# Kernel tuning notes

Measured on AMD Instinct MI355X. Metric: run time of the kernel, lower is better.

The kernel has to match this reference:

```python
import jax, jax.numpy as jnp
import numpy as np

B, S, H = 1, 4096, 2048
NH, NKV, HD = 8, 4, 256
I = 8192
EPS = 1e-6
THETA = 10000.0
WINDOW = 4096  # hardcoded sliding window for even layer_idx
LAYER_IDX = 0


def rms_norm(x, w):
    v = jnp.mean(jnp.square(x), axis=-1, keepdims=True)
    return x * jax.lax.rsqrt(v + EPS) * w


def rotate_half(x):
    h = x.shape[-1] // 2
    return jnp.concatenate([-x[..., h:], x[..., :h]], axis=-1)


def apply_rope(q, k, positions):
    # q: [B,S,NH,HD], k: [B,S,NKV,HD], positions: [B,S]
    inv_freq = 1.0 / (THETA ** (jnp.arange(0, HD, 2, dtype=jnp.float32) / HD))
    freqs = positions.astype(jnp.float32)[..., None] * inv_freq  # [B,S,HD/2]
    emb = jnp.concatenate([freqs, freqs], axis=-1)               # [B,S,HD]
    cos = jnp.cos(emb)[:, :, None, :]
    sin = jnp.sin(emb)[:, :, None, :]
    q = q * cos + rotate_half(q) * sin
    k = k * cos + rotate_half(k) * sin
    return q, k


def forward(hidden_states, q_w, k_w, v_w, o_w, gate_w, up_w, down_w, ln1_w, ln2_w,
            attention_mask, position_ids):
    # ---- input RMSNorm + attention ----
    residual = hidden_states
    x = rms_norm(hidden_states, ln1_w)

    q = (x @ q_w).reshape(B, S, NH, HD)
    k = (x @ k_w).reshape(B, S, NKV, HD)
    v = (x @ v_w).reshape(B, S, NKV, HD)
    q, k = apply_rope(q, k, position_ids)

    # GQA: repeat kv heads to match query heads
    groups = NH // NKV
    k = jnp.repeat(k, groups, axis=2)  # [B,S,NH,HD]
    v = jnp.repeat(v, groups, axis=2)

    # masks: padding mask AND causal AND (even layer) local window of WINDOW
    row = jnp.arange(S)[:, None]
    col = jnp.arange(S)[None, :]
    causal = col <= row                                   # [S,S]
    combined = causal[None, None] & (attention_mask[:, None, None, :] > 0)
    if LAYER_IDX % 2 == 0:
        keep = ~(col <= row - WINDOW)                     # mask out keys older than WINDOW
        combined = combined & keep[None, None]
    neg = jnp.finfo(jnp.float32).min
    bias = jnp.where(combined, 0.0, neg).astype(jnp.float32)  # [B,1,S,S]

    scale = HD ** -0.5
    scores = jnp.einsum('bqhd,bkhd->bhqk', q, k) * scale + bias
    probs = jax.nn.softmax(scores, axis=-1)
    attn = jnp.einsum('bhqk,bkhd->bqhd', probs, v).reshape(B, S, NH * HD)
    attn_out = attn @ o_w

    hidden_states = residual + attn_out

    # ---- post-attention RMSNorm + gated-GeLU MLP ----
    residual = hidden_states
    x = rms_norm(hidden_states, ln2_w)
    mlp = (jax.nn.gelu(x @ gate_w, approximate=True) * (x @ up_w)) @ down_w
    return residual + mlp


def setup_inputs() -> dict:
    key = jax.random.key(0)
    ks = jax.random.split(key, 9)
    std = 0.02
    n = lambda k, shp: jax.random.normal(k, shp, dtype=jnp.float32) * std
    return {
        'hidden_states': jax.random.normal(ks[0], (B, S, H), dtype=jnp.float32),
        'q_w': n(ks[1], (H, NH * HD)),
        'k_w': n(ks[2], (H, NKV * HD)),
        'v_w': n(ks[3], (H, NKV * HD)),
        'o_w': n(ks[4], (NH * HD, H)),
        'gate_w': n(ks[5], (H, I)),
        'up_w': n(ks[6], (H, I)),
        'down_w': n(ks[7], (I, H)),
        'ln1_w': jnp.ones((H,), jnp.float32),
        'ln2_w': jnp.ones((H,), jnp.float32),
        'attention_mask': jnp.ones((B, S), jnp.int32),
        'position_ids': jnp.broadcast_to(jnp.arange(S, dtype=jnp.int32)[None, :], (B, S)),
    }


def reference(hidden_states, q_w, k_w, v_w, o_w, gate_w, up_w, down_w, ln1_w, ln2_w,
              attention_mask, position_ids):
    return forward(hidden_states, q_w, k_w, v_w, o_w, gate_w, up_w, down_w,
                   ln1_w, ln2_w, attention_mask, position_ids)
```

## Files before the change

kernel.cpp:

```cpp
#include <hip/hip_runtime.h>
#include <hip/hip_bf16.h>
#include <math.h>

#define S_LEN 4096
#define HID   2048
#define NHEADS 8
#define NKVH   4
#define HDIM   256
#define FFN    8192
#define WIN    4096

typedef __bf16 bf16_t;
typedef __bf16 bf16x4 __attribute__((ext_vector_type(4)));
typedef __bf16 bf16x8 __attribute__((ext_vector_type(8)));
typedef float  floatx4 __attribute__((ext_vector_type(4)));

__device__ inline float waveReduceSum(float v) {
#pragma unroll
    for (int o = 32; o > 0; o >>= 1) v += __shfl_xor(v, o);
    return v;
}
__device__ inline float blockReduceSum(float v, float* sh) {
    int tid = threadIdx.x;
    v = waveReduceSum(v);
    if ((tid & 63) == 0) sh[tid >> 6] = v;
    __syncthreads();
    v = sh[0] + sh[1] + sh[2] + sh[3];
    __syncthreads();
    return v;
}

template <typename T>
__global__ __launch_bounds__(256) void transpose_bf16_kernel(const T* __restrict__ in,
                                                             bf16_t* __restrict__ out,
                                                             int R, int C) {
    __shared__ float tile[32][33];
    int tx = threadIdx.x & 31;
    int ty = threadIdx.x >> 5;
    int c0 = blockIdx.x * 32;
    int r0 = blockIdx.y * 32;
#pragma unroll
    for (int i = 0; i < 4; ++i)
        tile[ty + i * 8][tx] = (float)in[(long long)(r0 + ty + i * 8) * C + c0 + tx];
    __syncthreads();
#pragma unroll
    for (int i = 0; i < 4; ++i)
        out[(long long)(c0 + ty + i * 8) * R + r0 + tx] = (bf16_t)tile[tx][ty + i * 8];
}

__global__ __launch_bounds__(256) void rmsnorm_kernel(const float* __restrict__ x,
                                                      const float* __restrict__ w,
                                                      bf16_t* __restrict__ out) {
    __shared__ float sh[4];
    int row = blockIdx.x;
    const float* xr = x + (long long)row * HID;
    float v[8];
    float ss = 0.f;
#pragma unroll
    for (int i = 0; i < 8; ++i) {
        v[i] = xr[threadIdx.x + i * 256];
        ss += v[i] * v[i];
    }
    ss = blockReduceSum(ss, sh);
    float sc = rsqrtf(ss * (1.0f / HID) + 1e-6f);
#pragma unroll
    for (int i = 0; i < 8; ++i) {
        int c = threadIdx.x + i * 256;
        out[(long long)row * HID + c] = (bf16_t)(v[i] * sc * w[c]);
    }
}

__global__ __launch_bounds__(256) void rope_kernel(bf16_t* __restrict__ q,
                                                   bf16_t* __restrict__ k,
                                                   const int* __restrict__ pos_ids) {
    int s = blockIdx.x;
    float p = (float)pos_ids[s];
    for (int t = threadIdx.x; t < (NHEADS + NKVH) * (HDIM / 2); t += 256) {
        int head = t >> 7;
        int i = t & 127;
        float inv = expf(-(2.0f * (float)i / (float)HDIM) * 9.210340371976184f);
        float f = p * inv;
        float sn, cs;
        sincosf(f, &sn, &cs);
        bf16_t* base = (head < NHEADS) ? (q + (long long)s * HID + head * HDIM)
                                       : (k + (long long)s * (NKVH * HDIM) + (head - NHEADS) * HDIM);
        float a = (float)base[i];
        float b = (float)base[i + 128];
        base[i]       = (bf16_t)(a * cs - b * sn);
        base[i + 128] = (bf16_t)(b * cs + a * sn);
    }
}

__global__ __launch_bounds__(256) void flash_attn_kernel(const bf16_t* __restrict__ qg,
                                                         const bf16_t* __restrict__ kg,
                                                         const bf16_t* __restrict__ vTg,
                                                         bf16_t* __restrict__ op0,
                                                         bf16_t* __restrict__ op1,
                                                         float* __restrict__ mlb,
                                                         const int* __restrict__ amask) {
    __shared__ bf16_t sK[64 * 256];
    __shared__ bf16_t sV[256 * 64];

    const int h = blockIdx.y;
    const int kh = blockIdx.z;
    const int tid = threadIdx.x;
    const int lane = tid & 63;
    const int w = tid >> 6;
    const int tl = lane & 15;
    const int quad = lane >> 4;

    const bf16_t* Qh = qg + h * HDIM;
    const bf16_t* Kh = kg + (h >> 1) * HDIM;
    const bf16_t* Vh = vTg + (long long)(h >> 1) * HDIM * S_LEN;
    bf16_t* Op = kh ? op1 : op0;
    bf16_t* sP = sK + w * (16 * 72);

#pragma unroll 1
    for (int half = 0; half < 2; ++half) {
        const int qi = half ? (63 - blockIdx.x) : blockIdx.x;
        const int qr0 = qi * 64;
        const int ntiles = qi + 1;
        const int mid = ntiles >> 1;
        const int t0 = kh ? mid : 0;
        const int t1 = kh ? ntiles : mid;
        const int irow = qr0 + w * 16 + tl;

        const bf16_t* qrow = Qh + (long long)irow * HID;
        bf16x8 qf[8];
#pragma unroll
        for (int ks = 0; ks < 8; ++ks)
            qf[ks] = *(const bf16x8*)(qrow + (ks * 4 + quad) * 8);

        floatx4 oacc[16] = {};
        float m_i = -3e38f, l_i = 0.f;

        for (int t = t0; t < t1; ++t) {
            const int kt = t * 64;
#pragma unroll
            for (int it = 0; it < 8; ++it) {
                int s = it * 256 + tid;
                {
                    int m = s >> 5, sg = s & 31, g = sg ^ (m & 7);
                    const bf16_t* src = Kh + (long long)(kt + m) * (NKVH * HDIM) + g * 8;
                    __builtin_amdgcn_global_load_lds((const __attribute__((address_space(1))) void*)src,
                                                     (__attribute__((address_space(3))) void*)(sK + s * 8),
                                                     16, 0, 0);
                }
                {
                    int m = s >> 3, sg = s & 7, g = sg ^ (m & 7);
                    const bf16_t* src = Vh + (long long)m * S_LEN + kt + g * 8;
                    __builtin_amdgcn_global_load_lds((const __attribute__((address_space(1))) void*)src,
                                                     (__attribute__((address_space(3))) void*)(sV + s * 8),
                                                     16, 0, 0);
                }
            }
            __builtin_amdgcn_s_waitcnt(0x0f70);
            __syncthreads();

            floatx4 sacc[4] = {};
#pragma unroll
            for (int ks = 0; ks < 8; ++ks) {
                bf16x8 kf[4];
#pragma unroll
                for (int ni = 0; ni < 4; ++ni) {
                    int row = ni * 16 + tl;
                    int ph = (ks * 4 + quad) ^ (row & 7);
                    kf[ni] = *(const bf16x8*)(sK + row * 256 + ph * 8);
                }
#pragma unroll
                for (int ni = 0; ni < 4; ++ni)
                    sacc[ni] = __builtin_amdgcn_mfma_f32_16x16x32_bf16(kf[ni], qf[ks], sacc[ni], 0, 0, 0);
            }
            __syncthreads();

            float sv[4][4];
            float mx = -3e38f;
#pragma unroll
            for (int ni = 0; ni < 4; ++ni) {
                int4 am = *(const int4*)(amask + kt + ni * 16 + quad * 4);
#pragma unroll
                for (int r = 0; r < 4; ++r) {
                    int j = kt + ni * 16 + quad * 4 + r;
                    int amr = (r == 0) ? am.x : (r == 1) ? am.y : (r == 2) ? am.z : am.w;
                    bool valid = (j <= irow) && (j > irow - WIN) && (amr > 0);
                    float x = valid ? sacc[ni][r] * 0.0625f : -3e38f;
                    sv[ni][r] = x;
                    mx = fmaxf(mx, x);
                }
            }
            mx = fmaxf(mx, __shfl_xor(mx, 16));
            mx = fmaxf(mx, __shfl_xor(mx, 32));
            float mnew = fmaxf(m_i, mx);
            float alpha = __expf(m_i - mnew);
            float rs = 0.f;
#pragma unroll
            for (int ni = 0; ni < 4; ++ni) {
                bf16x4 pk;
#pragma unroll
                for (int r = 0; r < 4; ++r) {
                    float p = (sv[ni][r] > -1e37f) ? __expf(sv[ni][r] - mnew) : 0.f;
                    rs += p;
                    pk[r] = (bf16_t)p;
                }
                *(bf16x4*)(sP + tl * 72 + ni * 16 + quad * 4) = pk;
            }
            rs += __shfl_xor(rs, 16);
            rs += __shfl_xor(rs, 32);
            l_i = l_i * alpha + rs;
            m_i = mnew;

            floatx4 av;
#pragma unroll
            for (int r = 0; r < 4; ++r) av[r] = __shfl(alpha, quad * 4 + r);
#pragma unroll
            for (int dt = 0; dt < 16; ++dt) oacc[dt] *= av;

#pragma unroll
            for (int k2 = 0; k2 < 2; ++k2) {
                bf16x8 pf = *(const bf16x8*)(sP + tl * 72 + k2 * 32 + quad * 8);
#pragma unroll
                for (int dt = 0; dt < 16; ++dt) {
                    int d = dt * 16 + tl;
                    int ph = (k2 * 4 + quad) ^ (d & 7);
                    bf16x8 vf = *(const bf16x8*)(sV + d * 64 + ph * 8);
                    oacc[dt] = __builtin_amdgcn_mfma_f32_16x16x32_bf16(pf, vf, oacc[dt], 0, 0, 0);
                }
            }
            __syncthreads();
        }

        floatx4 inv;
#pragma unroll
        for (int r = 0; r < 4; ++r) {
            float lv = __shfl(l_i, quad * 4 + r);
            inv[r] = (lv > 0.f) ? 1.0f / lv : 0.f;
        }
#pragma unroll
        for (int dt = 0; dt < 16; ++dt) {
#pragma unroll
            for (int r = 0; r < 4; ++r) {
                long long row = qr0 + w * 16 + quad * 4 + r;
                Op[row * HID + h * HDIM + dt * 16 + tl] = (bf16_t)(oacc[dt][r] * inv[r]);
            }
        }
        if (quad == 0) {
            long long mi = ((long long)(kh * NHEADS + h) * S_LEN + qr0 + w * 16 + tl) * 2;
            mlb[mi] = m_i;
            mlb[mi + 1] = l_i;
        }
    }
}

__global__ __launch_bounds__(256) void combine_kernel(bf16_t* __restrict__ op0,
                                                      const bf16_t* __restrict__ op1,
                                                      const float* __restrict__ mlb) {
    int h = blockIdx.x;
    int row = blockIdx.y;
    int d = threadIdx.x;
    long long m0i = ((long long)h * S_LEN + row) * 2;
    long long m1i = ((long long)(NHEADS + h) * S_LEN + row) * 2;
    float m0 = mlb[m0i], l0 = mlb[m0i + 1];
    float m1 = mlb[m1i], l1 = mlb[m1i + 1];
    float M = fmaxf(m0, m1);
    float w0 = (l0 > 0.f) ? l0 * __expf(m0 - M) : 0.f;
    float w1 = (l1 > 0.f) ? l1 * __expf(m1 - M) : 0.f;
    float inv = 1.0f / (w0 + w1);
    long long idx = (long long)row * HID + h * HDIM + d;
    float v = (w0 * (float)op0[idx] + w1 * (float)op1[idx]) * inv;
    op0[idx] = (bf16_t)v;
}

template <int MODE>
__global__ __launch_bounds__(256) void gemm_kernel(const bf16_t* __restrict__ A, int lda,
                                                   const bf16_t* __restrict__ Bt, int ldb,
                                                   void* __restrict__ Cv, int ldc,
                                                   const void* __restrict__ aux, int K) {
    __shared__ bf16_t smem[2 * 128 * 64];
    bf16_t* sA = smem;
    bf16_t* sB = smem + 128 * 64;

    const int tid = threadIdx.x;
    const int n0 = blockIdx.x * 128;
    const int m0 = blockIdx.y * 128;

    const int lane = tid & 63;
    const int wid = tid >> 6;
    const int wm = (wid >> 1) * 64;
    const int wn = (wid & 1) * 64;
    const int tl = lane & 15;
    const int quad = lane >> 4;

    floatx4 acc[4][4] = {};

    for (int k0 = 0; k0 < K; k0 += 64) {
#pragma unroll
        for (int it = 0; it < 4; ++it) {
            int s = it * 256 + tid;
            int m = s >> 3;
            int sg = s & 7;
            int g = sg ^ (m & 7);
            const bf16_t* ga = A + (long long)(m0 + m) * lda + k0 + g * 8;
            __builtin_amdgcn_global_load_lds((const __attribute__((address_space(1))) void*)ga,
                                             (__attribute__((address_space(3))) void*)(sA + s * 8),
                                             16, 0, 0);
            const bf16_t* gb = Bt + (long long)(n0 + m) * ldb + k0 + g * 8;
            __builtin_amdgcn_global_load_lds((const __attribute__((address_space(1))) void*)gb,
                                             (__attribute__((address_space(3))) void*)(sB + s * 8),
                                             16, 0, 0);
        }
        __builtin_amdgcn_s_waitcnt(0x0f70);
        __syncthreads();

#pragma unroll
        for (int kk = 0; kk < 2; ++kk) {
            bf16x8 af[4], bfr[4];
#pragma unroll
            for (int mi = 0; mi < 4; ++mi) {
                int m = wm + mi * 16 + tl;
                int sg = (kk * 4 + quad) ^ (m & 7);
                af[mi] = *(const bf16x8*)(sA + m * 64 + sg * 8);
            }
#pragma unroll
            for (int ni = 0; ni < 4; ++ni) {
                int n = wn + ni * 16 + tl;
                int sg = (kk * 4 + quad) ^ (n & 7);
                bfr[ni] = *(const bf16x8*)(sB + n * 64 + sg * 8);
            }
#pragma unroll
            for (int mi = 0; mi < 4; ++mi)
#pragma unroll
                for (int ni = 0; ni < 4; ++ni)
                    acc[mi][ni] = __builtin_amdgcn_mfma_f32_16x16x32_bf16(af[mi], bfr[ni], acc[mi][ni], 0, 0, 0);
        }
        __syncthreads();
    }

#pragma unroll
    for (int mi = 0; mi < 4; ++mi) {
#pragma unroll
        for (int ni = 0; ni < 4; ++ni) {
#pragma unroll
            for (int r = 0; r < 4; ++r) {
                int gr = m0 + wm + mi * 16 + quad * 4 + r;
                int gc = n0 + wn + ni * 16 + tl;
                long long idx = (long long)gr * ldc + gc;
                float v = acc[mi][ni][r];
                if (MODE == 0) {
                    ((bf16_t*)Cv)[idx] = (bf16_t)v;
                } else if (MODE == 1) {
                    ((float*)Cv)[idx] = ((const float*)aux)[idx] + v;
                } else {
                    float g = (float)((const bf16_t*)aux)[idx];
                    float t = 0.7978845608028654f * (g + 0.044715f * g * g * g);
                    float ge = 0.5f * g * (1.0f + tanhf(t));
                    ((bf16_t*)Cv)[idx] = (bf16_t)(ge * v);
                }
            }
        }
    }
}

extern "C" void kernel_launch(void* const* d_in, const int* in_sizes, int n_in,
                              void* d_out, int out_size, void* d_ws, size_t ws_size,
                              hipStream_t stream) {
    const float* hidden = (const float*)d_in[0];
    const float* q_w    = (const float*)d_in[1];
    const float* k_w    = (const float*)d_in[2];
    const float* v_w    = (const float*)d_in[3];
    const float* o_w    = (const float*)d_in[4];
    const float* gate_w = (const float*)d_in[5];
    const float* up_w   = (const float*)d_in[6];
    const float* down_w = (const float*)d_in[7];
    const float* ln1_w  = (const float*)d_in[8];
    const float* ln2_w  = (const float*)d_in[9];
    const int* amask    = (const int*)d_in[10];
    const int* pos_ids  = (const int*)d_in[11];
    float* out = (float*)d_out;

    const size_t MB = 1ull << 20;
    char* ws = (char*)d_ws;
    bf16_t* wqT = (bf16_t*)(ws + 0 * MB);
    bf16_t* wkT = (bf16_t*)(ws + 8 * MB);
    bf16_t* wvT = (bf16_t*)(ws + 12 * MB);
    bf16_t* woT = (bf16_t*)(ws + 16 * MB);
    bf16_t* wgT = (bf16_t*)(ws + 24 * MB);
    bf16_t* wuT = (bf16_t*)(ws + 56 * MB);
    bf16_t* wdT = (bf16_t*)(ws + 88 * MB);
    bf16_t* xb    = (bf16_t*)(ws + 120 * MB);
    bf16_t* qb    = (bf16_t*)(ws + 136 * MB);
    bf16_t* kb    = (bf16_t*)(ws + 152 * MB);
    bf16_t* vb    = (bf16_t*)(ws + 160 * MB);
    bf16_t* vT    = (bf16_t*)(ws + 168 * MB);
    bf16_t* op0   = (bf16_t*)(ws + 120 * MB);
    bf16_t* op1   = (bf16_t*)(ws + 176 * MB);
    float*  mlb   = (float*) (ws + 192 * MB);
    bf16_t* attnb = (bf16_t*)(ws + 120 * MB);
    bf16_t* xb2   = (bf16_t*)(ws + 120 * MB);
    bf16_t* gateb = (bf16_t*)(ws + 136 * MB);
    (void)ws_size; (void)in_sizes; (void)n_in; (void)out_size;

    dim3 blk(256);

    transpose_bf16_kernel<float><<<dim3(64, 64), blk, 0, stream>>>(q_w, wqT, 2048, 2048);
    transpose_bf16_kernel<float><<<dim3(32, 64), blk, 0, stream>>>(k_w, wkT, 2048, 1024);
    transpose_bf16_kernel<float><<<dim3(32, 64), blk, 0, stream>>>(v_w, wvT, 2048, 1024);
    transpose_bf16_kernel<float><<<dim3(64, 64), blk, 0, stream>>>(o_w, woT, 2048, 2048);
    transpose_bf16_kernel<float><<<dim3(256, 64), blk, 0, stream>>>(gate_w, wgT, 2048, 8192);
    transpose_bf16_kernel<float><<<dim3(256, 64), blk, 0, stream>>>(up_w, wuT, 2048, 8192);
    transpose_bf16_kernel<float><<<dim3(64, 256), blk, 0, stream>>>(down_w, wdT, 8192, 2048);

    rmsnorm_kernel<<<dim3(S_LEN), blk, 0, stream>>>(hidden, ln1_w, xb);

    gemm_kernel<0><<<dim3(16, 32), blk, 0, stream>>>(xb, HID, wqT, HID, qb, 2048, nullptr, HID);
    gemm_kernel<0><<<dim3(8, 32), blk, 0, stream>>>(xb, HID, wkT, HID, kb, 1024, nullptr, HID);
    gemm_kernel<0><<<dim3(8, 32), blk, 0, stream>>>(xb, HID, wvT, HID, vb, 1024, nullptr, HID);

    rope_kernel<<<dim3(S_LEN), blk, 0, stream>>>(qb, kb, pos_ids);

    transpose_bf16_kernel<bf16_t><<<dim3(32, 128), blk, 0, stream>>>(vb, vT, S_LEN, 1024);

    flash_attn_kernel<<<dim3(32, NHEADS, 2), blk, 0, stream>>>(qb, kb, vT, op0, op1, mlb, amask);
    combine_kernel<<<dim3(NHEADS, S_LEN), blk, 0, stream>>>(op0, op1, mlb);

    gemm_kernel<1><<<dim3(16, 32), blk, 0, stream>>>(attnb, 2048, woT, 2048, out, 2048, hidden, 2048);

    rmsnorm_kernel<<<dim3(S_LEN), blk, 0, stream>>>(out, ln2_w, xb2);

    gemm_kernel<0><<<dim3(64, 32), blk, 0, stream>>>(xb2, HID, wgT, HID, gateb, FFN, nullptr, HID);
    gemm_kernel<2><<<dim3(64, 32), blk, 0, stream>>>(xb2, HID, wuT, HID, gateb, FFN, gateb, HID);
    gemm_kernel<1><<<dim3(16, 32), blk, 0, stream>>>(gateb, FFN, wdT, FFN, out, 2048, out, FFN);
}
```

Measured before the change: 1.316 ms.

## Register-prefetch next KV tile, lazy softmax rescale, and MFMA priority hints

Replaces the direct global-to-LDS loads with loads into registers that fetch the next K/V tile while the current tile is computed, then store it to LDS at the top of the next iteration. The P buffer moves into its own shared array so the mid-loop barrier can be dropped. Online-softmax rescaling of the output accumulators is skipped unless some row's max grows by more than a threshold of 8. s_setprio raises wave priority around the MFMA loops. The register staging adds VGPR pressure and extra LDS (which may lower occupancy), and the lazy rescale relies on exp(x - m) staying bounded in fp32/bf16.

Result: no change. 1.306 ms (-0.8%).

```diff
diff --git a/kernel.cpp b/kernel.cpp
--- a/kernel.cpp
+++ b/kernel.cpp
@@ -100,6 +100,7 @@
                                                          const int* __restrict__ amask) {
     __shared__ bf16_t sK[64 * 256];
     __shared__ bf16_t sV[256 * 64];
+    __shared__ bf16_t sPb[4 * 16 * 72];
 
     const int h = blockIdx.y;
     const int kh = blockIdx.z;
@@ -113,7 +114,7 @@
     const bf16_t* Kh = kg + (h >> 1) * HDIM;
     const bf16_t* Vh = vTg + (long long)(h >> 1) * HDIM * S_LEN;
     bf16_t* Op = kh ? op1 : op0;
-    bf16_t* sP = sK + w * (16 * 72);
+    bf16_t* sP = sPb + w * (16 * 72);
 
 #pragma unroll 1
     for (int half = 0; half < 2; ++half) {
@@ -134,30 +135,40 @@
         floatx4 oacc[16] = {};
         float m_i = -3e38f, l_i = 0.f;
 
-        for (int t = t0; t < t1; ++t) {
-            const int kt = t * 64;
+        bf16x8 stK[8], stV[8];
+        auto load_tile = [&](int kt) {
 #pragma unroll
             for (int it = 0; it < 8; ++it) {
                 int s = it * 256 + tid;
                 {
                     int m = s >> 5, sg = s & 31, g = sg ^ (m & 7);
-                    const bf16_t* src = Kh + (long long)(kt + m) * (NKVH * HDIM) + g * 8;
-                    __builtin_amdgcn_global_load_lds((const __attribute__((address_space(1))) void*)src,
-                                                     (__attribute__((address_space(3))) void*)(sK + s * 8),
-                                                     16, 0, 0);
+                    stK[it] = *(const bf16x8*)(Kh + (long long)(kt + m) * (NKVH * HDIM) + g * 8);
                 }
                 {
                     int m = s >> 3, sg = s & 7, g = sg ^ (m & 7);
-                    const bf16_t* src = Vh + (long long)m * S_LEN + kt + g * 8;
-                    __builtin_amdgcn_global_load_lds((const __attribute__((address_space(1))) void*)src,
-                                                     (__attribute__((address_space(3))) void*)(sV + s * 8),
-                                                     16, 0, 0);
-                }
-            }
-            __builtin_amdgcn_s_waitcnt(0x0f70);
+                    stV[it] = *(const bf16x8*)(Vh + (long long)m * S_LEN + kt + g * 8);
+                }
+            }
+        };
+
+        if (t0 < t1) load_tile(t0 * 64);
+
+#pragma unroll 1
+        for (int t = t0; t < t1; ++t) {
+            const int kt = t * 64;
+#pragma unroll
+            for (int it = 0; it < 8; ++it) {
+                int s = it * 256 + tid;
+                *(bf16x8*)(sK + s * 8) = stK[it];
+                *(bf16x8*)(sV + s * 8) = stV[it];
+            }
             __syncthreads();
 
+            if (t + 1 < t1) load_tile((t + 1) * 64);
+            __builtin_amdgcn_sched_barrier(0);
+
             floatx4 sacc[4] = {};
+            __builtin_amdgcn_s_setprio(1);
 #pragma unroll
             for (int ks = 0; ks < 8; ++ks) {
                 bf16x8 kf[4];
@@ -171,7 +182,7 @@
                 for (int ni = 0; ni < 4; ++ni)
                     sacc[ni] = __builtin_amdgcn_mfma_f32_16x16x32_bf16(kf[ni], qf[ks], sacc[ni], 0, 0, 0);
             }
-            __syncthreads();
+            __builtin_amdgcn_s_setprio(0);
 
             float sv[4][4];
             float mx = -3e38f;
@@ -190,8 +201,8 @@
             }
             mx = fmaxf(mx, __shfl_xor(mx, 16));
             mx = fmaxf(mx, __shfl_xor(mx, 32));
-            float mnew = fmaxf(m_i, mx);
-            float alpha = __expf(m_i - mnew);
+            bool noresc = __all(mx <= m_i + 8.0f);
+            float mnew = noresc ? m_i : fmaxf(m_i, mx);
             float rs = 0.f;
 #pragma unroll
             for (int ni = 0; ni < 4; ++ni) {
@@ -206,15 +217,20 @@
             }
             rs += __shfl_xor(rs, 16);
             rs += __shfl_xor(rs, 32);
-            l_i = l_i * alpha + rs;
-            m_i = mnew;
-
-            floatx4 av;
-#pragma unroll
-            for (int r = 0; r < 4; ++r) av[r] = __shfl(alpha, quad * 4 + r);
-#pragma unroll
-            for (int dt = 0; dt < 16; ++dt) oacc[dt] *= av;
-
+            if (noresc) {
+                l_i += rs;
+            } else {
+                float alpha = __expf(m_i - mnew);
+                l_i = l_i * alpha + rs;
+                m_i = mnew;
+                floatx4 av;
+#pragma unroll
+                for (int r = 0; r < 4; ++r) av[r] = __shfl(alpha, quad * 4 + r);
+#pragma unroll
+                for (int dt = 0; dt < 16; ++dt) oacc[dt] *= av;
+            }
+
+            __builtin_amdgcn_s_setprio(1);
 #pragma unroll
             for (int k2 = 0; k2 < 2; ++k2) {
                 bf16x8 pf = *(const bf16x8*)(sP + tl * 72 + k2 * 32 + quad * 8);
@@ -226,6 +242,7 @@
                     oacc[dt] = __builtin_amdgcn_mfma_f32_16x16x32_bf16(pf, vf, oacc[dt], 0, 0, 0);
                 }
             }
+            __builtin_amdgcn_s_setprio(0);
             __syncthreads();
         }
 
```
